# Kernel tuning notes

Hardware: AMD Instinct MI355X
Metric: run time of the kernel (lower is better)

Reference implementation:

```python
import jax, jax.numpy as jnp
import numpy as np

B, D, UNITS, NW = 64, 2048, 1024, 64  # batch, input_dim, units, n_weights


def _build_hash_indices(rng):
    """Replicates hash_matrix(): for each (unit j, bucket k), the (1-shifted)
    input positions i with hash(i,j) == k, padded with 0 (-> zero column)."""
    indx = rng.integers(0, NW, size=(D, UNITS))  # hash of (i, j) into [0, NW)
    counts = np.zeros((UNITS, NW), dtype=np.int64)
    for k in range(NW):
        counts[:, k] = (indx == k).sum(axis=0)
    L = int(counts.max())
    out = np.zeros((UNITS, NW, L), dtype=np.int64)
    for j in range(UNITS):
        col = indx[:, j]
        order = np.argsort(col, kind='stable')
        cnts = np.bincount(col, minlength=NW)
        splits = np.cumsum(cnts)[:-1]
        for k, part in enumerate(np.split(order, splits)):
            out[j, k, :len(part)] = part + 1  # +1 shift; 0 = padding
    return out


def setup_inputs() -> dict:
    key = jax.random.key(0)
    kx, kw = jax.random.split(key)
    x = jax.random.normal(kx, (B, D), dtype=jnp.float32)
    w = jax.random.normal(kw, (NW,), dtype=jnp.float32) * 0.05  # random_normal_initializer
    b = jnp.zeros((UNITS,), dtype=jnp.float32)
    indices = jnp.asarray(_build_hash_indices(np.random.default_rng(2)))
    return {"x": x, "w": w, "b": b, "indices": indices}


def reference(x, w, b, indices):
    # prepend a zero column so padding index 0 gathers 0.0
    x_cat = jnp.pad(x, ((0, 0), (1, 0)))                 # [B, D+1]
    gathered = jnp.take(x_cat, indices, axis=1)          # [B, UNITS, NW, L]
    reduced = gathered.sum(axis=-1)                      # [B, UNITS, NW]
    return jnp.einsum('buk,k->bu', reduced, w) + b       # [B, UNITS]
```

## Files before the change

kernel.cpp:

```cpp
#include <hip/hip_runtime.h>


#define B_DIM   64
#define D_DIM   2048
#define D4      (D_DIM / 4)
#define UNITS_N 1024
#define NW_N    64
#define U_PER_BLOCK 8
#define B_SPLIT 2
#define B_PER_BLOCK (B_DIM / B_SPLIT)
#define THREADS 1024
#define WAVES   (THREADS / 64)
#define PAIRS_PER_WAVE (U_PER_BLOCK * NW_N / WAVES)
#define ROWS_PER_WAVE  (B_PER_BLOCK / WAVES)
#define STEPS   (D4 / 64)

__global__ __launch_bounds__(THREADS)
void EfficientHashedLinear_72043781423546_kernel(
    const float* __restrict__ x,
    const float* __restrict__ w,
    const float* __restrict__ bias,
    const int*   __restrict__ indices,
    float*       __restrict__ out,
    int L)
{
    __shared__ float rows[U_PER_BLOCK][D_DIM];
    __shared__ float w_lds[NW_N];

    const int tid  = threadIdx.x;
    const int wave = tid >> 6;
    const int lane = tid & 63;
    const int u0   = blockIdx.x * U_PER_BLOCK;
    const int bh   = blockIdx.y;

    {
        float4* r4 = (float4*)rows;
        const float4 z = make_float4(0.f, 0.f, 0.f, 0.f);
        #pragma unroll
        for (int i = tid; i < U_PER_BLOCK * D4; i += THREADS)
            r4[i] = z;
        if (tid < NW_N) w_lds[tid] = w[tid];
    }

    int idxv[PAIRS_PER_WAVE];
    #pragma unroll
    for (int p = 0; p < PAIRS_PER_WAVE; ++p) {
        const int pair = wave * PAIRS_PER_WAVE + p;
        const int uu   = pair >> 6;
        const int k    = pair & 63;
        const int* bp  = indices + ((size_t)(u0 + uu) * NW_N + k) * L;
        idxv[p] = (lane < L) ? bp[lane] : 0;
    }

    __syncthreads();

    #pragma unroll
    for (int p = 0; p < PAIRS_PER_WAVE; ++p) {
        const int pair = wave * PAIRS_PER_WAVE + p;
        const int uu   = pair >> 6;
        const int k    = pair & 63;
        if (idxv[p] > 0) rows[uu][idxv[p] - 1] = w_lds[k];
    }
    if (L > 64) {
        #pragma unroll 1
        for (int p = 0; p < PAIRS_PER_WAVE; ++p) {
            const int pair = wave * PAIRS_PER_WAVE + p;
            const int uu   = pair >> 6;
            const int k    = pair & 63;
            const int* bp  = indices + ((size_t)(u0 + uu) * NW_N + k) * L;
            const float wk = w_lds[k];
            for (int l = 64 + lane; l < L; l += 64) {
                int idx = bp[l];
                if (idx > 0) rows[uu][idx - 1] = wk;
            }
        }
    }
    __syncthreads();

    const int b0 = bh * B_PER_BLOCK + wave * ROWS_PER_WAVE;
    const float4* x4 = (const float4*)x;

    float acc[ROWS_PER_WAVE][U_PER_BLOCK];
    #pragma unroll
    for (int bj = 0; bj < ROWS_PER_WAVE; ++bj)
        #pragma unroll
        for (int uu = 0; uu < U_PER_BLOCK; ++uu)
            acc[bj][uu] = 0.0f;

    #pragma unroll 1
    for (int step = 0; step < STEPS; ++step) {
        const int i4 = step * 64 + lane;
        float4 xv[ROWS_PER_WAVE];
        #pragma unroll
        for (int bj = 0; bj < ROWS_PER_WAVE; ++bj)
            xv[bj] = x4[(b0 + bj) * D4 + i4];
        #pragma unroll
        for (int uu = 0; uu < U_PER_BLOCK; ++uu) {
            const float4 rv = ((const float4*)rows[uu])[i4];
            #pragma unroll
            for (int bj = 0; bj < ROWS_PER_WAVE; ++bj) {
                acc[bj][uu] += xv[bj].x * rv.x;
                acc[bj][uu] += xv[bj].y * rv.y;
                acc[bj][uu] += xv[bj].z * rv.z;
                acc[bj][uu] += xv[bj].w * rv.w;
            }
        }
    }

    #pragma unroll
    for (int bj = 0; bj < ROWS_PER_WAVE; ++bj) {
        #pragma unroll
        for (int uu = 0; uu < U_PER_BLOCK; ++uu) {
            float v = acc[bj][uu];
            #pragma unroll
            for (int off = 32; off > 0; off >>= 1)
                v += __shfl_down(v, off, 64);
            if (lane == 0)
                out[(b0 + bj) * UNITS_N + (u0 + uu)] = v + bias[u0 + uu];
        }
    }
}

extern "C" void kernel_launch(void* const* d_in, const int* in_sizes, int n_in,
                              void* d_out, int out_size, void* d_ws, size_t ws_size,
                              hipStream_t stream) {
    const float* x       = (const float*)d_in[0];
    const float* w       = (const float*)d_in[1];
    const float* bias    = (const float*)d_in[2];
    const int*   indices = (const int*)d_in[3];
    float*       out     = (float*)d_out;

    const int L = in_sizes[3] / (UNITS_N * NW_N);

    dim3 grid(UNITS_N / U_PER_BLOCK, B_SPLIT);
    dim3 block(THREADS);
    EfficientHashedLinear_72043781423546_kernel<<<grid, block, 0, stream>>>(
        x, w, bias, indices, out, L);
}
```

Before: 80.12 us.

## Split hashed weight scatter into a separate kernel that builds dense W

Splits the work into two kernels when a workspace is available. The first scatters the hashed weights once into a dense global matrix W of size UNITS x D; the second loads W rows into LDS and runs the same dot-product loop. Before, every block zeroed LDS and scattered the indices itself, and with the batch split of two that scatter ran twice per unit group. In exchange the new path adds a second launch, scattered 4-byte global writes and a round trip of an 8 MB matrix through global memory. It depends on every input position being covered by exactly one bucket, because W is never zeroed.

```diff
diff --git a/kernel.cpp b/kernel.cpp
--- a/kernel.cpp
+++ b/kernel.cpp
@@ -15,6 +15,93 @@
 #define ROWS_PER_WAVE  (B_PER_BLOCK / WAVES)
 #define STEPS   (D4 / 64)
 
+__global__ __launch_bounds__(256)
+void EfficientHashedLinear_72043781423546_buildW(
+    const float* __restrict__ w,
+    const int*   __restrict__ indices,
+    float*       __restrict__ W,
+    int L)
+{
+    const int bucket = blockIdx.x * 4 + (threadIdx.x >> 6);
+    const int lane   = threadIdx.x & 63;
+    const int u      = bucket >> 6;
+    const int k      = bucket & 63;
+    const float wk   = w[k];
+    const int* bp    = indices + (size_t)bucket * L;
+    for (int l = lane; l < L; l += 64) {
+        const int idx = bp[l];
+        if (idx > 0) W[(size_t)u * D_DIM + idx - 1] = wk;
+    }
+}
+
+__global__ __launch_bounds__(THREADS)
+void EfficientHashedLinear_72043781423546_gemm(
+    const float* __restrict__ x,
+    const float* __restrict__ W,
+    const float* __restrict__ bias,
+    float*       __restrict__ out)
+{
+    __shared__ float rows[U_PER_BLOCK][D_DIM];
+
+    const int tid  = threadIdx.x;
+    const int wave = tid >> 6;
+    const int lane = tid & 63;
+    const int u0   = blockIdx.x * U_PER_BLOCK;
+    const int bh   = blockIdx.y;
+
+    {
+        const float4* g4 = (const float4*)(W + (size_t)u0 * D_DIM);
+        float4* r4 = (float4*)rows;
+        #pragma unroll
+        for (int i = tid; i < U_PER_BLOCK * D4; i += THREADS)
+            r4[i] = g4[i];
+    }
+    __syncthreads();
+
+    const int b0 = bh * B_PER_BLOCK + wave * ROWS_PER_WAVE;
+    const float4* x4 = (const float4*)x;
+
+    float acc[ROWS_PER_WAVE][U_PER_BLOCK];
+    #pragma unroll
+    for (int bj = 0; bj < ROWS_PER_WAVE; ++bj)
+        #pragma unroll
+        for (int uu = 0; uu < U_PER_BLOCK; ++uu)
+            acc[bj][uu] = 0.0f;
+
+    #pragma unroll 1
+    for (int step = 0; step < STEPS; ++step) {
+        const int i4 = step * 64 + lane;
+        float4 xv[ROWS_PER_WAVE];
+        #pragma unroll
+        for (int bj = 0; bj < ROWS_PER_WAVE; ++bj)
+            xv[bj] = x4[(b0 + bj) * D4 + i4];
+        #pragma unroll
+        for (int uu = 0; uu < U_PER_BLOCK; ++uu) {
+            const float4 rv = ((const float4*)rows[uu])[i4];
+            #pragma unroll
+            for (int bj = 0; bj < ROWS_PER_WAVE; ++bj) {
+                acc[bj][uu] += xv[bj].x * rv.x;
+                acc[bj][uu] += xv[bj].y * rv.y;
+                acc[bj][uu] += xv[bj].z * rv.z;
+                acc[bj][uu] += xv[bj].w * rv.w;
+            }
+        }
+    }
+
+    #pragma unroll
+    for (int bj = 0; bj < ROWS_PER_WAVE; ++bj) {
+        #pragma unroll
+        for (int uu = 0; uu < U_PER_BLOCK; ++uu) {
+            float v = acc[bj][uu];
+            #pragma unroll
+            for (int off = 32; off > 0; off >>= 1)
+                v += __shfl_down(v, off, 64);
+            if (lane == 0)
+                out[(b0 + bj) * UNITS_N + (u0 + uu)] = v + bias[u0 + uu];
+        }
+    }
+}
+
 __global__ __launch_bounds__(THREADS)
 void EfficientHashedLinear_72043781423546_kernel(
     const float* __restrict__ x,
@@ -131,9 +218,19 @@
     float*       out     = (float*)d_out;
 
     const int L = in_sizes[3] / (UNITS_N * NW_N);
-
-    dim3 grid(UNITS_N / U_PER_BLOCK, B_SPLIT);
-    dim3 block(THREADS);
-    EfficientHashedLinear_72043781423546_kernel<<<grid, block, 0, stream>>>(
-        x, w, bias, indices, out, L);
-}
+    const size_t Wbytes = (size_t)UNITS_N * D_DIM * sizeof(float);
+
+    if (ws_size >= Wbytes && d_ws != nullptr) {
+        float* W = (float*)d_ws;
+        EfficientHashedLinear_72043781423546_buildW<<<
+            dim3(UNITS_N * NW_N / 4), dim3(256), 0, stream>>>(w, indices, W, L);
+        EfficientHashedLinear_72043781423546_gemm<<<
+            dim3(UNITS_N / U_PER_BLOCK, B_SPLIT), dim3(THREADS), 0, stream>>>(
+            x, W, bias, out);
+    } else {
+        dim3 grid(UNITS_N / U_PER_BLOCK, B_SPLIT);
+        dim3 block(THREADS);
+        EfficientHashedLinear_72043781423546_kernel<<<grid, block, 0, stream>>>(
+            x, w, bias, indices, out, L);
+    }
+}
```

Measured after the change: 92.80 us. 1.16x slower.
